# Optimization experiments

Hardware: AMD Instinct MI355X
Metric: run time of the kernel (lower is better)

The kernel has to match this reference:

```python
import jax, jax.numpy as jnp
import numpy as np

B, T, J = 256, 150, 25  # batch, time_step, num_joints (NTU-style skeleton)
K_LIST = (2, 3, 4)      # k values from the source loop -> 3 stats each -> topo_feat_dim = 9


def setup_inputs() -> dict:
    key = jax.random.key(0)
    x = jax.random.normal(key, (B, T, J, 3), dtype=jnp.float32)
    return {"x": x}


def _pairwise_dist(pos):
    # pos: [B,T,J,3] -> dist: [B,T,J,J], safe sqrt so grad at zero diagonal is 0
    diff = pos[:, :, :, None, :] - pos[:, :, None, :, :]          # [B,T,J,J,3]
    s = jnp.sum(diff * diff, axis=-1)                              # [B,T,J,J]
    return jnp.where(s > 0, jnp.sqrt(jnp.where(s > 0, s, 1.0)), 0.0)


def reference(x) -> jnp.ndarray:
    # Faithful, fully vectorized version of the topo-feature block of
    # FiveStreamMaha_GCN_Model.forward (per-frame cdist + kNN + stats),
    # batched over all frames instead of Python loops over t and k.
    pos = x[..., :3]                     # [B,T,J,3]
    dist = _pairwise_dist(pos)           # [B,T,J,J]

    feats = []
    for k in K_LIST:
        actual_k = min(k, J - 1)
        # smallest (actual_k+1) distances; drop self (distance 0 at index 0)
        neg_vals, _ = jax.lax.top_k(-dist, actual_k + 1)   # [B,T,J,k+1], descending in -d
        knn_d = -neg_vals[..., 1:actual_k + 1]             # [B,T,J,k], ascending distances
        avg_dist = jnp.mean(knn_d, axis=-1)                # [B,T,J]
        std_dist = jnp.std(knn_d, axis=-1, ddof=1)         # torch.std default: unbiased
        min_dist = jnp.min(knn_d, axis=-1)                 # [B,T,J]
        k_feat = jnp.stack([avg_dist, std_dist, min_dist], axis=-1)  # [B,T,J,3]
        feats.append(jnp.mean(k_feat, axis=1))             # mean over time -> [B,J,3]

    return jnp.concatenate(feats, axis=-1)                 # [B,J,9]
```

## Files before the change

kernel.cpp:

```cpp
#include <hip/hip_runtime.h>
#include <cfloat>

#define NB 256
#define NT 150
#define NJ 25
#define CHUNK 10
#define CPB (NT / CHUNK)
#define WAVES 4
#define BLOCKSZ 256
#define NW (NB * CPB)

#define INS4(s0, s1, s2, s3, v)                                   \
    {                                                             \
        float m_;                                                 \
        m_ = fminf(s0, v); v = fmaxf(s0, v); s0 = m_;             \
        m_ = fminf(s1, v); v = fmaxf(s1, v); s1 = m_;             \
        m_ = fminf(s2, v); v = fmaxf(s2, v); s2 = m_;             \
        s3 = fminf(s3, v);                                        \
    }

__global__ __launch_bounds__(BLOCKSZ) void knn_partial_kernel(
        const float* __restrict__ x, float* __restrict__ ws) {
    __shared__ float4 spos[WAVES][CHUNK][NJ];

    const int tid  = threadIdx.x;
    const int wave = tid >> 6;
    const int lane = tid & 63;
    const int half = lane >> 5;
    const int jj   = lane & 31;
    const bool act = (jj < NJ);

    const int gw = blockIdx.x * WAVES + wave;
    const int b  = gw / CPB;
    const int c  = gw - b * CPB;
    const int t0 = c * CHUNK;

    const float* src = x + (size_t)(b * NT + t0) * NJ * 3;
    for (int p = lane; p < CHUNK * NJ; p += 64) {
        const int f = p / NJ;
        const int j = p - f * NJ;
        const float* s = src + p * 3;
        spos[wave][f][j] = make_float4(s[0], s[1], s[2], 0.0f);
    }
    __syncthreads();

    float acc[9];
#pragma unroll
    for (int f = 0; f < 9; ++f) acc[f] = 0.0f;

    for (int p = 0; p < CHUNK / 2; ++p) {
        const int fr = 2 * p + half;

        const float4 own = spos[wave][fr][act ? jj : 0];

        float4 q[NJ];
#pragma unroll
        for (int i = 0; i < NJ; ++i) q[i] = spos[wave][fr][i];

        float a0 = FLT_MAX, a1 = FLT_MAX, a2 = FLT_MAX, a3 = FLT_MAX;
        float e0 = FLT_MAX, e1 = FLT_MAX, e2 = FLT_MAX, e3 = FLT_MAX;
#pragma unroll
        for (int i = 0; i < 13; ++i) {
            const float dx = q[i].x - own.x, dy = q[i].y - own.y, dz = q[i].z - own.z;
            float d2 = dx * dx + dy * dy + dz * dz;
            d2 = (i == jj) ? FLT_MAX : d2;
            INS4(a0, a1, a2, a3, d2);
        }
#pragma unroll
        for (int i = 13; i < NJ; ++i) {
            const float dx = q[i].x - own.x, dy = q[i].y - own.y, dz = q[i].z - own.z;
            float d2 = dx * dx + dy * dy + dz * dz;
            d2 = (i == jj) ? FLT_MAX : d2;
            INS4(e0, e1, e2, e3, d2);
        }
        const float l0 = fminf(a0, e3), l1 = fminf(a1, e2);
        const float l2 = fminf(a2, e1), l3 = fminf(a3, e0);
        const float m0 = fminf(l0, l2), m2 = fmaxf(l0, l2);
        const float m1 = fminf(l1, l3), m3 = fmaxf(l1, l3);
        const float r0 = fminf(m0, m1), r1 = fmaxf(m0, m1);
        const float r2 = fminf(m2, m3), r3 = fmaxf(m2, m3);

        const float d1 = sqrtf(r0), d2r = sqrtf(r1), d3 = sqrtf(r2), d4 = sqrtf(r3);

        const float s2 = d1 + d2r, a2f = 0.5f * s2;
        float u1 = d1 - a2f, u2 = d2r - a2f;
        acc[0] += a2f; acc[1] += sqrtf(u1 * u1 + u2 * u2); acc[2] += d1;
        const float s3 = s2 + d3, a3f = s3 * (1.0f / 3.0f);
        u1 = d1 - a3f; u2 = d2r - a3f; float u3 = d3 - a3f;
        acc[3] += a3f; acc[4] += sqrtf((u1 * u1 + u2 * u2 + u3 * u3) * 0.5f); acc[5] += d1;
        const float s4 = s3 + d4, a4f = 0.25f * s4;
        u1 = d1 - a4f; u2 = d2r - a4f; u3 = d3 - a4f; const float u4 = d4 - a4f;
        acc[6] += a4f;
        acc[7] += sqrtf((u1 * u1 + u2 * u2 + u3 * u3 + u4 * u4) * (1.0f / 3.0f));
        acc[8] += d1;
    }

#pragma unroll
    for (int f = 0; f < 9; ++f) acc[f] += __shfl_xor(acc[f], 32, 64);

    if (act && half == 0) {
        float* op = ws + (size_t)gw * 225;
#pragma unroll
        for (int f = 0; f < 9; ++f) op[f * NJ + jj] = acc[f];
    }
}

__global__ __launch_bounds__(BLOCKSZ) void reduce_kernel(
        const float* __restrict__ ws, float* __restrict__ out) {
    const int i = blockIdx.x * blockDim.x + threadIdx.x;
    if (i >= NB * NJ * 9) return;
    const int b = i / 225;
    const int r = i - b * 225;
    float s = 0.0f;
#pragma unroll
    for (int c = 0; c < CPB; ++c) s += ws[(size_t)(b * CPB + c) * 225 + r];
    const int f = r / NJ;
    const int j = r - f * NJ;
    out[b * 225 + j * 9 + f] = s * (1.0f / (float)NT);
}

extern "C" void kernel_launch(void* const* d_in, const int* in_sizes, int n_in,
                              void* d_out, int out_size, void* d_ws, size_t ws_size,
                              hipStream_t stream) {
    const float* x = (const float*)d_in[0];
    float* out = (float*)d_out;
    float* ws = (float*)d_ws;

    knn_partial_kernel<<<NW / WAVES, BLOCKSZ, 0, stream>>>(x, ws);
    reduce_kernel<<<(NB * NJ * 9 + BLOCKSZ - 1) / BLOCKSZ, BLOCKSZ, 0, stream>>>(ws, out);
}
```

Measured before the change: 78.18 us.

## Shrink time chunk, use hardware sqrt, load neighbors per iteration, reformulate variance

Cuts the per-wave frame chunk from 10 to 6, which launches more waves. It adds a min-blocks launch bound and keeps the frame loop rolled. It reads neighbour positions from shared memory inside the distance loop instead of preloading 25 float4 registers, which lowers register pressure. It swaps sqrtf for the raw AMDGPU sqrt builtin and computes the std through the sum-of-squares identity with a clamp at zero, which saves arithmetic but can lose precision to cancellation.

```diff
diff --git a/kernel.cpp b/kernel.cpp
--- a/kernel.cpp
+++ b/kernel.cpp
@@ -4,11 +4,13 @@
 #define NB 256
 #define NT 150
 #define NJ 25
-#define CHUNK 10
+#define CHUNK 6
 #define CPB (NT / CHUNK)
 #define WAVES 4
 #define BLOCKSZ 256
 #define NW (NB * CPB)
+
+#define FSQRT(x) __builtin_amdgcn_sqrtf(x)
 
 #define INS4(s0, s1, s2, s3, v)                                   \
     {                                                             \
@@ -19,7 +21,7 @@
         s3 = fminf(s3, v);                                        \
     }
 
-__global__ __launch_bounds__(BLOCKSZ) void knn_partial_kernel(
+__global__ __launch_bounds__(BLOCKSZ, 4) void knn_partial_kernel(
         const float* __restrict__ x, float* __restrict__ ws) {
     __shared__ float4 spos[WAVES][CHUNK][NJ];
 
@@ -48,27 +50,25 @@
 #pragma unroll
     for (int f = 0; f < 9; ++f) acc[f] = 0.0f;
 
+#pragma unroll 1
     for (int p = 0; p < CHUNK / 2; ++p) {
         const int fr = 2 * p + half;
-
         const float4 own = spos[wave][fr][act ? jj : 0];
-
-        float4 q[NJ];
-#pragma unroll
-        for (int i = 0; i < NJ; ++i) q[i] = spos[wave][fr][i];
 
         float a0 = FLT_MAX, a1 = FLT_MAX, a2 = FLT_MAX, a3 = FLT_MAX;
         float e0 = FLT_MAX, e1 = FLT_MAX, e2 = FLT_MAX, e3 = FLT_MAX;
 #pragma unroll
         for (int i = 0; i < 13; ++i) {
-            const float dx = q[i].x - own.x, dy = q[i].y - own.y, dz = q[i].z - own.z;
+            const float4 q = spos[wave][fr][i];
+            const float dx = q.x - own.x, dy = q.y - own.y, dz = q.z - own.z;
             float d2 = dx * dx + dy * dy + dz * dz;
             d2 = (i == jj) ? FLT_MAX : d2;
             INS4(a0, a1, a2, a3, d2);
         }
 #pragma unroll
         for (int i = 13; i < NJ; ++i) {
-            const float dx = q[i].x - own.x, dy = q[i].y - own.y, dz = q[i].z - own.z;
+            const float4 q = spos[wave][fr][i];
+            const float dx = q.x - own.x, dy = q.y - own.y, dz = q.z - own.z;
             float d2 = dx * dx + dy * dy + dz * dz;
             d2 = (i == jj) ? FLT_MAX : d2;
             INS4(e0, e1, e2, e3, d2);
@@ -80,18 +80,21 @@
         const float r0 = fminf(m0, m1), r1 = fmaxf(m0, m1);
         const float r2 = fminf(m2, m3), r3 = fmaxf(m2, m3);
 
-        const float d1 = sqrtf(r0), d2r = sqrtf(r1), d3 = sqrtf(r2), d4 = sqrtf(r3);
+        const float d1 = FSQRT(r0), d2r = FSQRT(r1);
+        const float d3 = FSQRT(r2), d4 = FSQRT(r3);
 
+        const float rs2 = r0 + r1, rs3 = rs2 + r2, rs4 = rs3 + r3;
         const float s2 = d1 + d2r, a2f = 0.5f * s2;
-        float u1 = d1 - a2f, u2 = d2r - a2f;
-        acc[0] += a2f; acc[1] += sqrtf(u1 * u1 + u2 * u2); acc[2] += d1;
+        acc[0] += a2f;
+        acc[1] += FSQRT(fmaxf(rs2 - 2.0f * a2f * a2f, 0.0f));
+        acc[2] += d1;
         const float s3 = s2 + d3, a3f = s3 * (1.0f / 3.0f);
-        u1 = d1 - a3f; u2 = d2r - a3f; float u3 = d3 - a3f;
-        acc[3] += a3f; acc[4] += sqrtf((u1 * u1 + u2 * u2 + u3 * u3) * 0.5f); acc[5] += d1;
+        acc[3] += a3f;
+        acc[4] += FSQRT(fmaxf((rs3 - 3.0f * a3f * a3f) * 0.5f, 0.0f));
+        acc[5] += d1;
         const float s4 = s3 + d4, a4f = 0.25f * s4;
-        u1 = d1 - a4f; u2 = d2r - a4f; u3 = d3 - a4f; const float u4 = d4 - a4f;
         acc[6] += a4f;
-        acc[7] += sqrtf((u1 * u1 + u2 * u2 + u3 * u3 + u4 * u4) * (1.0f / 3.0f));
+        acc[7] += FSQRT(fmaxf((rs4 - 4.0f * a4f * a4f) * (1.0f / 3.0f), 0.0f));
         acc[8] += d1;
     }
 
```

Result: faster. 76.26 us (-2.5%).
